# Kernel optimization log

Measured on AMD Instinct MI355X. Metric: run time of the kernel, lower is better.

The kernel has to match this reference:

```python
import jax, jax.numpy as jnp
import numpy as np


def setup_inputs() -> dict:
    key = jax.random.key(0)
    k_u, k_lam, k_B, k_C = jax.random.split(key, 4)
    batch, seq_len, d_model, N = 4, 4096, 1024, 64
    return {
        "u": jax.random.normal(k_u, (batch, seq_len, d_model), dtype=jnp.float32),
        "Lambda": jax.random.normal(k_lam, (N,), dtype=jnp.float32),
        "log_dt": jnp.zeros((1,), dtype=jnp.float32),
        "B": jax.random.normal(k_B, (N, d_model), dtype=jnp.float32),
        "C": jax.random.normal(k_C, (d_model, N), dtype=jnp.float32),
        "D": jnp.zeros((d_model,), dtype=jnp.float32),
    }


def reference(u, Lambda, log_dt, B, C, D):
    # dt = exp(log_dt); A = diag(exp(dt * (-exp(Lambda)))) -> diagonal decay vector a of shape (N,)
    dt = jnp.exp(log_dt)          # (1,)
    a = jnp.exp(-dt * jnp.exp(Lambda))  # (N,)

    # Precompute input projection for all timesteps: Bu[b, t, n] = u[b, t] @ B.T
    Bu = jnp.einsum("bld,nd->bln", u, B)  # (batch, L, N)

    # Sequential diagonal recurrence: x_t = a * x_{t-1} + Bu_t
    def step(x, bu_t):
        x = a * x + bu_t
        return x, x

    x0 = jnp.zeros((u.shape[0], Lambda.shape[0]), dtype=u.dtype)
    _, xs = jax.lax.scan(step, x0, jnp.swapaxes(Bu, 0, 1))  # xs: (L, batch, N)
    xs = jnp.swapaxes(xs, 0, 1)  # (batch, L, N)

    # Output projection + skip: y_t = x_t @ C.T + D * u_t
    return jnp.einsum("bln,dn->bld", xs, C) + D * u
```

## Files before the change

### kernel.cpp

```cpp
#include <hip/hip_runtime.h>
#include <hip/hip_bf16.h>


constexpr int BATCH  = 4;
constexpr int L      = 4096;
constexpr int DM     = 1024;
constexpr int N      = 64;
constexpr int ROWS   = BATCH * L;
constexpr int CHUNK  = 64;
constexpr int NCHUNK = L / CHUNK;

typedef __attribute__((ext_vector_type(8))) short     bf16x8;
typedef __attribute__((ext_vector_type(4))) float     f32x4;

__device__ __forceinline__ unsigned int pk2(float x, float y) {
  __hip_bfloat162 h = __float22bfloat162_rn(make_float2(x, y));
  return *reinterpret_cast<unsigned int*>(&h);
}

__global__ __launch_bounds__(256) void bu_scan(const float* __restrict__ u,
                                               const float* __restrict__ Bm,
                                               const float* __restrict__ Lambda,
                                               const float* __restrict__ log_dt,
                                               unsigned short* __restrict__ xsb,
                                               float* __restrict__ F) {
  __shared__ __align__(16) char smem[36864];
  typedef unsigned short HalfT[64][72];
  HalfT* As = reinterpret_cast<HalfT*>(smem);
  HalfT* Bs = reinterpret_cast<HalfT*>(smem + 18432);
  float (*T)[68] = reinterpret_cast<float (*)[68]>(smem);
  float* W = reinterpret_cast<float*>(smem + 17408);

  const int tid  = threadIdx.x;
  const int lane = tid & 63;
  const int wv   = tid >> 6;
  const int l15  = lane & 15;
  const int g    = lane >> 4;
  const int row0 = blockIdx.x * 64;

  const int sr = tid >> 4;
  const int sq = tid & 15;

  f32x4 acc[4] = {};
  float4 pa[2][4], pb[2][4];

  constexpr int NCH = DM / 64;
  #pragma unroll
  for (int s = 0; s < 2; ++s) {
    const int kb = s * 64;
    #pragma unroll
    for (int i = 0; i < 4; ++i) {
      const int r = sr + i * 16;
      pa[s][i] = *reinterpret_cast<const float4*>(&u[(long)(row0 + r) * DM + kb + sq * 4]);
      pb[s][i] = *reinterpret_cast<const float4*>(&Bm[(long)r * DM + kb + sq * 4]);
    }
  }

  #pragma unroll
  for (int c = 0; c < NCH; ++c) {
    const int s = c & 1;
    if (c) __syncthreads();
    #pragma unroll
    for (int i = 0; i < 4; ++i) {
      const int r = sr + i * 16;
      uint2 ha = {pk2(pa[s][i].x, pa[s][i].y), pk2(pa[s][i].z, pa[s][i].w)};
      uint2 hb = {pk2(pb[s][i].x, pb[s][i].y), pk2(pb[s][i].z, pb[s][i].w)};
      *reinterpret_cast<uint2*>(&As[s][r][sq * 4]) = ha;
      *reinterpret_cast<uint2*>(&Bs[s][r][sq * 4]) = hb;
    }
    __syncthreads();
    if (c + 2 < NCH) {
      const int kb = (c + 2) * 64;
      #pragma unroll
      for (int i = 0; i < 4; ++i) {
        const int r = sr + i * 16;
        pa[s][i] = *reinterpret_cast<const float4*>(&u[(long)(row0 + r) * DM + kb + sq * 4]);
        pb[s][i] = *reinterpret_cast<const float4*>(&Bm[(long)r * DM + kb + sq * 4]);
      }
    }
    #pragma unroll
    for (int ks = 0; ks < 2; ++ks) {
      const bf16x8 af = *reinterpret_cast<const bf16x8*>(
          &As[s][wv * 16 + l15][ks * 32 + g * 8]);
      #pragma unroll
      for (int t = 0; t < 4; ++t) {
        const bf16x8 bfr = *reinterpret_cast<const bf16x8*>(
            &Bs[s][t * 16 + l15][ks * 32 + g * 8]);
        acc[t] = __builtin_amdgcn_mfma_f32_16x16x32_bf16(af, bfr, acc[t], 0, 0, 0);
      }
    }
  }

  __syncthreads();
  #pragma unroll
  for (int t = 0; t < 4; ++t)
    #pragma unroll
    for (int r = 0; r < 4; ++r)
      T[wv * 16 + g * 4 + r][t * 16 + l15] = acc[t][r];
  __syncthreads();

  const float dtv = __expf(log_dt[0]);
  const float wn  = -dtv * __expf(Lambda[lane]);
  const float a   = __expf(wn);
  const float a16 = __expf(wn * 16.0f);

  float p[16];
  {
    float x = 0.0f;
    #pragma unroll
    for (int j = 0; j < 16; ++j) { x = fmaf(a, x, T[wv * 16 + j][lane]); p[j] = x; }
    W[wv * 64 + lane] = x;
  }
  __syncthreads();
  float P = 0.0f;
  #pragma unroll
  for (int w2 = 0; w2 < 3; ++w2)
    if (w2 < wv) P = fmaf(a16, P, W[w2 * 64 + lane]);
  __syncthreads();
  float cfac = P;
  #pragma unroll
  for (int j = 0; j < 16; ++j) { cfac *= a; T[wv * 16 + j][lane] = p[j] + cfac; }
  if (wv == 3) F[blockIdx.x * N + lane] = p[15] + cfac;
  __syncthreads();

  #pragma unroll
  for (int i = 0; i < 4; ++i) {
    const int idx = tid + i * 256;
    const int r = idx >> 4, q = idx & 15;
    const float4 v = *reinterpret_cast<const float4*>(&T[r][q * 4]);
    uint2 o = {pk2(v.x, v.y), pk2(v.z, v.w)};
    *reinterpret_cast<uint2*>(&xsb[(long)(row0 + r) * N + q * 4]) = o;
  }
}

__global__ __launch_bounds__(256) void y_gemm(const unsigned short* __restrict__ xsb,
                                              const float* __restrict__ F,
                                              const float* __restrict__ Lambda,
                                              const float* __restrict__ log_dt,
                                              const float* __restrict__ Cm,
                                              const float* __restrict__ Dv,
                                              const float* __restrict__ u,
                                              float* __restrict__ y) {
  __shared__ __align__(16) char smem[33792];
  unsigned short (*Xs)[72] = reinterpret_cast<unsigned short (*)[72]>(smem);
  unsigned short (*Cs)[72] = reinterpret_cast<unsigned short (*)[72]>(smem + 9216);
  float (*T)[132] = reinterpret_cast<float (*)[132]>(smem);
  __shared__ float ciS[64], wS[64], Dsh[128];

  const int tid  = threadIdx.x;
  const int lane = tid & 63;
  const int wv   = tid >> 6;
  const int l15  = lane & 15;
  const int g    = lane >> 4;
  const int row0 = (blockIdx.x & 255) * 64;
  const int d0   = (blockIdx.x >> 8) * 128;
  const int b    = row0 >> 12;
  const int c    = (row0 >> 6) & 63;

  if (tid < 64) {
    const int n = tid;
    const float dtv = __expf(log_dt[0]);
    const float wn  = -dtv * __expf(Lambda[n]);
    wS[n] = wn;
    const float aS = __expf(wn * 64.0f);
    float P = 0.0f;
    int j = 0;
    for (; j + 16 <= c; j += 16) {
      float fj[16];
      #pragma unroll
      for (int k = 0; k < 16; ++k) fj[k] = F[((b << 6) + j + k) * N + n];
      #pragma unroll
      for (int k = 0; k < 16; ++k) P = fmaf(aS, P, fj[k]);
    }
    for (; j < c; ++j) P = fmaf(aS, P, F[((b << 6) + j) * N + n]);
    ciS[n] = P;
  } else if (tid < 192) {
    Dsh[tid - 64] = Dv[d0 + (tid - 64)];
  }
  __syncthreads();

  #pragma unroll
  for (int i = 0; i < 2; ++i) {
    const int idx = tid + i * 256;
    const int r = idx >> 3, q = idx & 7;
    const uint4 xv = *reinterpret_cast<const uint4*>(&xsb[(long)(row0 + r) * N + q * 8]);
    const float rp1 = (float)(r + 1);
    float f[8];
    #pragma unroll
    for (int j = 0; j < 4; ++j) {
      const unsigned int wbits = (&xv.x)[j];
      f[2 * j]     = __uint_as_float(wbits << 16);
      f[2 * j + 1] = __uint_as_float(wbits & 0xFFFF0000u);
    }
    #pragma unroll
    for (int j = 0; j < 8; ++j) {
      const int n = q * 8 + j;
      f[j] = fmaf(__expf(wS[n] * rp1), ciS[n], f[j]);
    }
    uint4 o = {pk2(f[0], f[1]), pk2(f[2], f[3]), pk2(f[4], f[5]), pk2(f[6], f[7])};
    *reinterpret_cast<uint4*>(&Xs[r][q * 8]) = o;
  }
  #pragma unroll
  for (int i = 0; i < 8; ++i) {
    const int idx = tid + i * 256;
    const int r = idx >> 4, q = idx & 15;
    const float4 v = *reinterpret_cast<const float4*>(&Cm[(long)(d0 + r) * N + q * 4]);
    uint2 o = {pk2(v.x, v.y), pk2(v.z, v.w)};
    *reinterpret_cast<uint2*>(&Cs[r][q * 4]) = o;
  }
  __syncthreads();

  bf16x8 af[2];
  #pragma unroll
  for (int ks = 0; ks < 2; ++ks)
    af[ks] = *reinterpret_cast<const bf16x8*>(&Xs[wv * 16 + l15][ks * 32 + g * 8]);

  f32x4 acc[8] = {};
  #pragma unroll
  for (int t = 0; t < 8; ++t) {
    #pragma unroll
    for (int ks = 0; ks < 2; ++ks) {
      const bf16x8 bfr = *reinterpret_cast<const bf16x8*>(
          &Cs[t * 16 + l15][ks * 32 + g * 8]);
      acc[t] = __builtin_amdgcn_mfma_f32_16x16x32_bf16(af[ks], bfr, acc[t], 0, 0, 0);
    }
  }

  __syncthreads();
  #pragma unroll
  for (int t = 0; t < 8; ++t)
    #pragma unroll
    for (int r = 0; r < 4; ++r)
      T[wv * 16 + g * 4 + r][t * 16 + l15] = acc[t][r];
  __syncthreads();

  #pragma unroll
  for (int i = 0; i < 8; ++i) {
    const int id = tid + i * 256;
    const int r = id >> 5;
    const int q = id & 31;
    float4 v = *reinterpret_cast<const float4*>(&T[r][q * 4]);
    const float4 dd = *reinterpret_cast<const float4*>(&Dsh[q * 4]);
    if (dd.x != 0.0f || dd.y != 0.0f || dd.z != 0.0f || dd.w != 0.0f) {
      const float4 uu = *reinterpret_cast<const float4*>(
          &u[(long)(row0 + r) * DM + d0 + q * 4]);
      v.x = fmaf(dd.x, uu.x, v.x);
      v.y = fmaf(dd.y, uu.y, v.y);
      v.z = fmaf(dd.z, uu.z, v.z);
      v.w = fmaf(dd.w, uu.w, v.w);
    }
    *reinterpret_cast<float4*>(&y[(long)(row0 + r) * DM + d0 + q * 4]) = v;
  }
}

extern "C" void kernel_launch(void* const* d_in, const int* in_sizes, int n_in,
                              void* d_out, int out_size, void* d_ws, size_t ws_size,
                              hipStream_t stream) {
  const float* u      = (const float*)d_in[0];
  const float* Lambda = (const float*)d_in[1];
  const float* log_dt = (const float*)d_in[2];
  const float* Bm     = (const float*)d_in[3];
  const float* Cm     = (const float*)d_in[4];
  const float* Dv     = (const float*)d_in[5];
  float* y = (float*)d_out;

  const size_t planeB = (size_t)ROWS * N;
  unsigned short* xsb = (unsigned short*)d_ws;
  float* F = (float*)(xsb + planeB);

  bu_scan<<<ROWS / 64, 256, 0, stream>>>(u, Bm, Lambda, log_dt, xsb, F);
  y_gemm<<<(ROWS / 64) * (DM / 128), 256, 0, stream>>>(xsb, F, Lambda, log_dt,
                                                       Cm, Dv, u, y);
}
```

Measured before the change: 36.24 us.

## Shrink y_gemm tile to 64 columns and store MFMA results directly

Halves the output-column tile of the y projection kernel from 128 to 64, doubling the grid, and swaps the MFMA operands so C supplies the A fragment and the state supplies B. Each lane's accumulator then maps to four contiguous output columns, so results are written to global memory directly as float4 instead of being staged through a shared-memory transpose. The first barrier is moved after the bf16 unpack to overlap global loads with the decay-prefix computation. In exchange, the per-block prefix recomputation (ciS loop over F) and the state-tile conversion are repeated twice as often, and the direct stores are less coalesced, with 16-byte pieces spread across rows.

```diff
diff --git a/kernel.cpp b/kernel.cpp
--- a/kernel.cpp
+++ b/kernel.cpp
@@ -141,11 +141,9 @@
                                               const float* __restrict__ Dv,
                                               const float* __restrict__ u,
                                               float* __restrict__ y) {
-  __shared__ __align__(16) char smem[33792];
-  unsigned short (*Xs)[72] = reinterpret_cast<unsigned short (*)[72]>(smem);
-  unsigned short (*Cs)[72] = reinterpret_cast<unsigned short (*)[72]>(smem + 9216);
-  float (*T)[132] = reinterpret_cast<float (*)[132]>(smem);
-  __shared__ float ciS[64], wS[64], Dsh[128];
+  __shared__ __align__(16) unsigned short Xs[64][72];
+  __shared__ __align__(16) unsigned short Cs[64][72];
+  __shared__ float ciS[64], wS[64], Dsh[64];
 
   const int tid  = threadIdx.x;
   const int lane = tid & 63;
@@ -153,7 +151,7 @@
   const int l15  = lane & 15;
   const int g    = lane >> 4;
   const int row0 = (blockIdx.x & 255) * 64;
-  const int d0   = (blockIdx.x >> 8) * 128;
+  const int d0   = (blockIdx.x >> 8) * 64;
   const int b    = row0 >> 12;
   const int c    = (row0 >> 6) & 63;
 
@@ -174,10 +172,9 @@
     }
     for (; j < c; ++j) P = fmaf(aS, P, F[((b << 6) + j) * N + n]);
     ciS[n] = P;
-  } else if (tid < 192) {
+  } else if (tid < 128) {
     Dsh[tid - 64] = Dv[d0 + (tid - 64)];
   }
-  __syncthreads();
 
   #pragma unroll
   for (int i = 0; i < 2; ++i) {
@@ -192,6 +189,7 @@
       f[2 * j]     = __uint_as_float(wbits << 16);
       f[2 * j + 1] = __uint_as_float(wbits & 0xFFFF0000u);
     }
+    if (i == 0) __syncthreads();
     #pragma unroll
     for (int j = 0; j < 8; ++j) {
       const int n = q * 8 + j;
@@ -201,7 +199,7 @@
     *reinterpret_cast<uint4*>(&Xs[r][q * 8]) = o;
   }
   #pragma unroll
-  for (int i = 0; i < 8; ++i) {
+  for (int i = 0; i < 4; ++i) {
     const int idx = tid + i * 256;
     const int r = idx >> 4, q = idx & 15;
     const float4 v = *reinterpret_cast<const float4*>(&Cm[(long)(d0 + r) * N + q * 4]);
@@ -210,46 +208,37 @@
   }
   __syncthreads();
 
-  bf16x8 af[2];
-  #pragma unroll
-  for (int ks = 0; ks < 2; ++ks)
-    af[ks] = *reinterpret_cast<const bf16x8*>(&Xs[wv * 16 + l15][ks * 32 + g * 8]);
-
-  f32x4 acc[8] = {};
-  #pragma unroll
-  for (int t = 0; t < 8; ++t) {
-    #pragma unroll
-    for (int ks = 0; ks < 2; ++ks) {
-      const bf16x8 bfr = *reinterpret_cast<const bf16x8*>(
-          &Cs[t * 16 + l15][ks * 32 + g * 8]);
-      acc[t] = __builtin_amdgcn_mfma_f32_16x16x32_bf16(af[ks], bfr, acc[t], 0, 0, 0);
-    }
-  }
-
-  __syncthreads();
-  #pragma unroll
-  for (int t = 0; t < 8; ++t)
-    #pragma unroll
-    for (int r = 0; r < 4; ++r)
-      T[wv * 16 + g * 4 + r][t * 16 + l15] = acc[t][r];
-  __syncthreads();
-
-  #pragma unroll
-  for (int i = 0; i < 8; ++i) {
-    const int id = tid + i * 256;
-    const int r = id >> 5;
-    const int q = id & 31;
-    float4 v = *reinterpret_cast<const float4*>(&T[r][q * 4]);
-    const float4 dd = *reinterpret_cast<const float4*>(&Dsh[q * 4]);
-    if (dd.x != 0.0f || dd.y != 0.0f || dd.z != 0.0f || dd.w != 0.0f) {
-      const float4 uu = *reinterpret_cast<const float4*>(
-          &u[(long)(row0 + r) * DM + d0 + q * 4]);
+  bf16x8 af[2], bft[4][2];
+  #pragma unroll
+  for (int ks = 0; ks < 2; ++ks) {
+    af[ks] = *reinterpret_cast<const bf16x8*>(&Cs[wv * 16 + l15][ks * 32 + g * 8]);
+    #pragma unroll
+    for (int tt = 0; tt < 4; ++tt)
+      bft[tt][ks] = *reinterpret_cast<const bf16x8*>(&Xs[tt * 16 + l15][ks * 32 + g * 8]);
+  }
+
+  f32x4 acc[4] = {};
+  #pragma unroll
+  for (int tt = 0; tt < 4; ++tt)
+    #pragma unroll
+    for (int ks = 0; ks < 2; ++ks)
+      acc[tt] = __builtin_amdgcn_mfma_f32_16x16x32_bf16(af[ks], bft[tt][ks], acc[tt], 0, 0, 0);
+
+  const int dcol = d0 + wv * 16 + g * 4;
+  const float4 dd = *reinterpret_cast<const float4*>(&Dsh[wv * 16 + g * 4]);
+  const bool dnz = (dd.x != 0.0f || dd.y != 0.0f || dd.z != 0.0f || dd.w != 0.0f);
+  #pragma unroll
+  for (int tt = 0; tt < 4; ++tt) {
+    const long row = row0 + tt * 16 + l15;
+    float4 v = {acc[tt][0], acc[tt][1], acc[tt][2], acc[tt][3]};
+    if (dnz) {
+      const float4 uu = *reinterpret_cast<const float4*>(&u[row * DM + dcol]);
       v.x = fmaf(dd.x, uu.x, v.x);
       v.y = fmaf(dd.y, uu.y, v.y);
       v.z = fmaf(dd.z, uu.z, v.z);
       v.w = fmaf(dd.w, uu.w, v.w);
     }
-    *reinterpret_cast<float4*>(&y[(long)(row0 + r) * DM + d0 + q * 4]) = v;
+    *reinterpret_cast<float4*>(&y[row * DM + dcol]) = v;
   }
 }
 
@@ -269,6 +258,6 @@
   float* F = (float*)(xsb + planeB);
 
   bu_scan<<<ROWS / 64, 256, 0, stream>>>(u, Bm, Lambda, log_dt, xsb, F);
-  y_gemm<<<(ROWS / 64) * (DM / 128), 256, 0, stream>>>(xsb, F, Lambda, log_dt,
-                                                       Cm, Dv, u, y);
-}
+  y_gemm<<<(ROWS / 64) * (DM / 64), 256, 0, stream>>>(xsb, F, Lambda, log_dt,
+                                                      Cm, Dv, u, y);
+}
```

Result: slower. 40.45 us (+11.6%).
